# Kernel tuning notes

Measured on AMD Instinct MI355X. Metric: run time of the kernel, lower is better.

## Reference

```python
import jax, jax.numpy as jnp
import numpy as np

CODEBOOK_SIZE = 8192
D_MODEL = 256
COMMITMENT_COST = 0.25


def setup_inputs() -> dict:
    key = jax.random.key(0)
    k1, k2 = jax.random.split(key)
    z = jax.random.normal(k1, (16, 512, D_MODEL), dtype=jnp.float32)
    # uniform(-1/K, 1/K) init like the torch module
    codebook = jax.random.uniform(
        k2, (CODEBOOK_SIZE, D_MODEL), dtype=jnp.float32,
        minval=-1.0 / CODEBOOK_SIZE, maxval=1.0 / CODEBOOK_SIZE)
    return {"z": z, "codebook": codebook}


def reference(z, codebook):
    B, P, D = z.shape
    flat = z.reshape(-1, D)  # [N, D]
    distances = (jnp.sum(flat * flat, axis=1, keepdims=True)
                 + jnp.sum(codebook * codebook, axis=1)
                 - 2.0 * jnp.matmul(flat, codebook.T))
    indices = jnp.argmin(distances, axis=1)  # [N] int
    quantized = codebook[indices]            # [N, D] gather
    # non-EMA VQ loss: codebook loss + commitment loss
    e_latent_loss = jnp.mean((jax.lax.stop_gradient(quantized) - flat) ** 2)
    q_latent_loss = jnp.mean((quantized - jax.lax.stop_gradient(flat)) ** 2)
    loss = q_latent_loss + COMMITMENT_COST * e_latent_loss
    # straight-through estimator
    quantized_st = flat + jax.lax.stop_gradient(quantized - flat)
    return (loss, quantized_st.reshape(B, P, D), indices.reshape(B, P))
```

## Files before the change

### kernel.cpp

```cpp
#include <hip/hip_runtime.h>
#include <hip/hip_bf16.h>
#include <math.h>


#define NROWS 8192
#define DDIM  256
#define KCW   8192
#define CAP   128
#define MARGIN 5e-4f

typedef __attribute__((ext_vector_type(8))) short short8;
typedef __attribute__((ext_vector_type(4))) float f32x4;
typedef unsigned int u32;

__device__ inline void async_copy16(void* lds_uniform, const void* gsrc) {
  __builtin_amdgcn_global_load_lds(
      (const __attribute__((address_space(1))) u32*)gsrc,
      (__attribute__((address_space(3))) u32*)lds_uniform, 16, 0, 0);
}

__device__ inline unsigned fmap(float f) {
  unsigned b = __float_as_uint(f);
  return (b & 0x80000000u) ? ~b : (b | 0x80000000u);
}
__device__ inline float funmap(unsigned u) {
  unsigned b = (u & 0x80000000u) ? (u & 0x7FFFFFFFu) : ~u;
  return __uint_as_float(b);
}

__global__ __launch_bounds__(256) void k_prep_cast(const float* __restrict__ z,
                                                   const float* __restrict__ cb,
                                                   ushort* __restrict__ zb,
                                                   ushort* __restrict__ cbb,
                                                   float* __restrict__ e2f,
                                                   unsigned* __restrict__ rowMinU,
                                                   unsigned* __restrict__ cnt) {
  int t = threadIdx.x, w = t >> 6, lane = t & 63;
  int wid = blockIdx.x * 4 + w;
  bool isCb = wid >= NROWS;
  int row = isCb ? wid - NROWS : wid;
  const float* src = (isCb ? cb : z) + (size_t)row * DDIM + lane * 4;
  float4 v = *reinterpret_cast<const float4*>(src);
  ushort4 o;
  __hip_bfloat16 bx = __float2bfloat16(v.x); o.x = *(ushort*)&bx;
  __hip_bfloat16 by = __float2bfloat16(v.y); o.y = *(ushort*)&by;
  __hip_bfloat16 bz = __float2bfloat16(v.z); o.z = *(ushort*)&bz;
  __hip_bfloat16 bw = __float2bfloat16(v.w); o.w = *(ushort*)&bw;
  ushort* dst = (isCb ? cbb : zb) + (size_t)row * DDIM + lane * 4;
  *reinterpret_cast<ushort4*>(dst) = o;
  if (isCb) {
    double d = (double)v.x * v.x + (double)v.y * v.y + (double)v.z * v.z + (double)v.w * v.w;
#pragma unroll
    for (int off = 1; off < 64; off <<= 1) d += __shfl_xor(d, off);
    if (lane == 0) e2f[row] = (float)d;
  } else {
    if (lane == 0) { rowMinU[row] = ~0u; cnt[row] = 0; }
  }
}

__global__ __launch_bounds__(256) void k_score1(const ushort* __restrict__ zb,
                                                const ushort* __restrict__ cbb,
                                                const float* __restrict__ e2f,
                                                unsigned* __restrict__ rowMinU,
                                                unsigned* __restrict__ cnt,
                                                ushort* __restrict__ cand) {
  __shared__ ushort Ab[128 * 64];
  __shared__ ushort Bb[128 * 64];
  int t = threadIdx.x, w = t >> 6, lane = t & 63;
  int wg = ((blockIdx.x & 7) << 9) | (blockIdx.x >> 3);
  int mt = wg >> 6, nt = wg & 63;
  int wm = w >> 1, wn = w & 1;
  int cl = lane & 15, g = lane >> 4;

  int rloc8 = lane >> 3;
  int sslot = (lane & 7) ^ rloc8;
  const ushort* arow_base = zb  + (size_t)(mt * 128) * DDIM;
  const ushort* brow_base = cbb + (size_t)(nt * 128) * DDIM;

  f32x4 acc[4][4];
#pragma unroll
  for (int m = 0; m < 4; ++m)
#pragma unroll
    for (int n = 0; n < 4; ++n) acc[m][n] = (f32x4){0.f, 0.f, 0.f, 0.f};

  for (int ks = 0; ks < 4; ++ks) {
#pragma unroll
    for (int i = 0; i < 8; ++i) {
      int ch = w * 8 + i;
      int ct = ch & 15;
      int row = ct * 8 + rloc8;
      const ushort* src = (ch < 16)
          ? arow_base + (size_t)row * DDIM + ks * 64 + sslot * 8
          : brow_base + (size_t)row * DDIM + ks * 64 + sslot * 8;
      char* ldsb = (char*)(ch < 16 ? Ab : Bb) + ct * 1024;
      async_copy16(ldsb, src);
    }
    __syncthreads();
#pragma unroll
    for (int kk = 0; kk < 2; ++kk) {
      short8 af[4], bf[4];
#pragma unroll
      for (int m = 0; m < 4; ++m) {
        int arow = wm * 64 + m * 16 + cl;
        int ab = arow * 128 + (((kk * 4 + g) ^ (arow & 7)) << 4);
        af[m] = *reinterpret_cast<const short8*>((char*)Ab + ab);
      }
#pragma unroll
      for (int n = 0; n < 4; ++n) {
        int brow = wn * 64 + n * 16 + cl;
        int bb = brow * 128 + (((kk * 4 + g) ^ (brow & 7)) << 4);
        bf[n] = *reinterpret_cast<const short8*>((char*)Bb + bb);
      }
#pragma unroll
      for (int m = 0; m < 4; ++m)
#pragma unroll
        for (int n = 0; n < 4; ++n)
          acc[m][n] = __builtin_amdgcn_mfma_f32_16x16x32_bf16(af[m], bf[n], acc[m][n], 0, 0, 0);
    }
    __syncthreads();
  }

  int col_base = nt * 128 + wn * 64;
  int row_base = mt * 128 + wm * 64;
  float e2v[4];
#pragma unroll
  for (int n = 0; n < 4; ++n) e2v[n] = e2f[col_base + n * 16 + cl];

#pragma unroll
  for (int m = 0; m < 4; ++m) {
#pragma unroll
    for (int j = 0; j < 4; ++j) {
      int row = row_base + m * 16 + g * 4 + j;
      float s0 = __fsub_rn(e2v[0], __fmul_rn(2.0f, acc[m][0][j]));
      float s1 = __fsub_rn(e2v[1], __fmul_rn(2.0f, acc[m][1][j]));
      float s2 = __fsub_rn(e2v[2], __fmul_rn(2.0f, acc[m][2][j]));
      float s3 = __fsub_rn(e2v[3], __fmul_rn(2.0f, acc[m][3][j]));
      float mn = fminf(fminf(s0, s1), fminf(s2, s3));
#pragma unroll
      for (int off = 1; off < 16; off <<= 1)
        mn = fminf(mn, __shfl_xor(mn, off));
      float thr;
      if (cl == 0) {
        unsigned old = atomicMin(&rowMinU[row], fmap(mn));
        thr = fminf(funmap(old), mn) + MARGIN;
      }
      thr = __shfl(thr, g << 4);
      if (s0 <= thr) { unsigned sl = atomicAdd(&cnt[row], 1u); if (sl < CAP) cand[(size_t)row * CAP + sl] = (ushort)(col_base + 0 * 16 + cl); }
      if (s1 <= thr) { unsigned sl = atomicAdd(&cnt[row], 1u); if (sl < CAP) cand[(size_t)row * CAP + sl] = (ushort)(col_base + 1 * 16 + cl); }
      if (s2 <= thr) { unsigned sl = atomicAdd(&cnt[row], 1u); if (sl < CAP) cand[(size_t)row * CAP + sl] = (ushort)(col_base + 2 * 16 + cl); }
      if (s3 <= thr) { unsigned sl = atomicAdd(&cnt[row], 1u); if (sl < CAP) cand[(size_t)row * CAP + sl] = (ushort)(col_base + 3 * 16 + cl); }
    }
  }
}

__global__ __launch_bounds__(256) void k_rescore_gather(const float* __restrict__ z,
                                                        const float* __restrict__ cb,
                                                        const float* __restrict__ e2f,
                                                        const unsigned* __restrict__ cnt,
                                                        const ushort* __restrict__ cand,
                                                        float* __restrict__ out_q,
                                                        float* __restrict__ out_idx,
                                                        float* __restrict__ lpart) {
  int t = threadIdx.x, w = t >> 6, lane = t & 63;
  int row = blockIdx.x * 4 + w;
  const float* xp = z + (size_t)row * DDIM;
  const float4* xp4 = reinterpret_cast<const float4*>(xp);
  float4 x4 = xp4[lane];
  double rd = (double)x4.x * x4.x + (double)x4.y * x4.y + (double)x4.z * x4.z + (double)x4.w * x4.w;
#pragma unroll
  for (int off = 1; off < 64; off <<= 1) rd += __shfl_xor(rd, off);
  float r2v = (float)rd;

  unsigned n = cnt[row];
  float s = INFINITY; int ci = 0x7fffffff;
  if (n <= CAP) {
#pragma unroll
    for (int base = 0; base < CAP; base += 64) {
      int k_i = base + lane;
      if (k_i < (int)n) {
        int c = cand[(size_t)row * CAP + k_i];
        const float4* ep4 = reinterpret_cast<const float4*>(cb + (size_t)c * DDIM);
        float acc = 0.f;
#pragma unroll 4
        for (int k4 = 0; k4 < 64; ++k4) {
          float4 e = ep4[k4], x = xp4[k4];
          acc = __fmaf_rn(x.x, e.x, acc);
          acc = __fmaf_rn(x.y, e.y, acc);
          acc = __fmaf_rn(x.z, e.z, acc);
          acc = __fmaf_rn(x.w, e.w, acc);
        }
        float scv = __fsub_rn(__fadd_rn(r2v, e2f[c]), __fmul_rn(2.0f, acc));
        if (scv < s || (scv == s && c < ci)) { s = scv; ci = c; }
      }
    }
  } else {
    for (int base = 0; base < KCW; base += 64) {
      int c = base + lane;
      const float4* ep4 = reinterpret_cast<const float4*>(cb + (size_t)c * DDIM);
      float acc = 0.f;
#pragma unroll 4
      for (int k4 = 0; k4 < 64; ++k4) {
        float4 e = ep4[k4], x = xp4[k4];
        acc = __fmaf_rn(x.x, e.x, acc);
        acc = __fmaf_rn(x.y, e.y, acc);
        acc = __fmaf_rn(x.z, e.z, acc);
        acc = __fmaf_rn(x.w, e.w, acc);
      }
      float scv = __fsub_rn(__fadd_rn(r2v, e2f[c]), __fmul_rn(2.0f, acc));
      if (scv < s) { s = scv; ci = c; }
    }
  }
#pragma unroll
  for (int off = 1; off < 64; off <<= 1) {
    float os = __shfl_xor(s, off); int oi = __shfl_xor(ci, off);
    if (os < s || (os == s && oi < ci)) { s = os; ci = oi; }
  }
  if (lane == 0) out_idx[row] = (float)ci;

  float4 qv = *reinterpret_cast<const float4*>(cb + (size_t)ci * DDIM + lane * 4);
  float* o = out_q + (size_t)row * DDIM + lane * 4;
  o[0] = qv.x; o[1] = qv.y; o[2] = qv.z; o[3] = qv.w;
  float dx = qv.x - x4.x, dy = qv.y - x4.y, dz = qv.z - x4.z, dw = qv.w - x4.w;
  double d = (double)dx * dx + (double)dy * dy + (double)dz * dz + (double)dw * dw;
#pragma unroll
  for (int off = 1; off < 64; off <<= 1) d += __shfl_xor(d, off);
  if (lane == 0) lpart[row] = (float)d;
}

__global__ __launch_bounds__(256) void k_loss(const float* __restrict__ lpart,
                                              float* __restrict__ out0) {
  __shared__ double red[256];
  int t = threadIdx.x;
  double s = 0.0;
  for (int j = t; j < NROWS; j += 256) s += lpart[j];
  red[t] = s;
  __syncthreads();
  for (int off = 128; off > 0; off >>= 1) {
    if (t < off) red[t] += red[t + off];
    __syncthreads();
  }
  if (t == 0) out0[0] = (float)(1.25 * red[0] / (double)((size_t)NROWS * DDIM));
}

extern "C" void kernel_launch(void* const* d_in, const int* in_sizes, int n_in,
                              void* d_out, int out_size, void* d_ws, size_t ws_size,
                              hipStream_t stream) {
  const float* z  = (const float*)d_in[0];
  const float* cb = (const float*)d_in[1];
  float* out = (float*)d_out;
  char* ws = (char*)d_ws;
  const size_t HALF = (size_t)NROWS * DDIM;

  ushort* zb  = (ushort*)(out + 4);
  ushort* cbb = zb + HALF;

  size_t off = 0;
  float*    e2f     = (float*)(ws + off);    off += NROWS * 4;
  unsigned* cnt     = (unsigned*)(ws + off); off += NROWS * 4;
  unsigned* rowMinU = (unsigned*)(ws + off);
  float*    lpart   = (float*)(ws + off);    off += NROWS * 4;
  ushort*   cand    = (ushort*)(ws + off);   off += (size_t)NROWS * CAP * 2;

  float* out_q   = out + 1;
  float* out_idx = out + 1 + HALF;

  k_prep_cast     <<<(2 * NROWS) / 4, 256, 0, stream>>>(z, cb, zb, cbb, e2f, rowMinU, cnt);
  k_score1        <<<64 * 64,         256, 0, stream>>>(zb, cbb, e2f, rowMinU, cnt, cand);
  k_rescore_gather<<<NROWS / 4,       256, 0, stream>>>(z, cb, e2f, cnt, cand, out_q, out_idx, lpart);
  k_loss          <<<1,               256, 0, stream>>>(lpart, out);
}
```

Before: 246.3 us.

## Split scoring into exact-min pass and candidate-filter pass to shrink rescore work

Replaces the single scoring kernel, which used a running atomic minimum, with two passes over the bf16 distance GEMM. The first pass computes each row's exact approximate minimum and the second collects only candidates within a margin of it. This gives far fewer candidates, so the cap drops to 56 and the fp32 rescore runs as a single per-lane pass. The K-tile also grows to 128 with larger LDS buffers and launch bounds of 2. The cost is running the GEMM twice, in exchange for less atomic contention and a much cheaper rescore.

```diff
diff --git a/kernel.cpp b/kernel.cpp
--- a/kernel.cpp
+++ b/kernel.cpp
@@ -6,8 +6,8 @@
 #define NROWS 8192
 #define DDIM  256
 #define KCW   8192
-#define CAP   128
-#define MARGIN 5e-4f
+#define CAP   56
+#define MARGIN 8e-4f
 
 typedef __attribute__((ext_vector_type(8))) short short8;
 typedef __attribute__((ext_vector_type(4))) float f32x4;
@@ -54,26 +54,27 @@
     for (int off = 1; off < 64; off <<= 1) d += __shfl_xor(d, off);
     if (lane == 0) e2f[row] = (float)d;
   } else {
-    if (lane == 0) { rowMinU[row] = ~0u; cnt[row] = 0; }
-  }
-}
-
-__global__ __launch_bounds__(256) void k_score1(const ushort* __restrict__ zb,
-                                                const ushort* __restrict__ cbb,
-                                                const float* __restrict__ e2f,
-                                                unsigned* __restrict__ rowMinU,
-                                                unsigned* __restrict__ cnt,
-                                                ushort* __restrict__ cand) {
-  __shared__ ushort Ab[128 * 64];
-  __shared__ ushort Bb[128 * 64];
+    if (lane == 0) { rowMinU[row] = 0xFF800000u; cnt[row] = 0; }
+  }
+}
+
+template<int PHASE>
+__global__ __launch_bounds__(256, 2) void k_score(const ushort* __restrict__ zb,
+                                                  const ushort* __restrict__ cbb,
+                                                  const float* __restrict__ e2f,
+                                                  unsigned* __restrict__ rowMinU,
+                                                  unsigned* __restrict__ cnt,
+                                                  int* __restrict__ cand) {
+  __shared__ ushort Ab[128 * 128];
+  __shared__ ushort Bb[128 * 128];
   int t = threadIdx.x, w = t >> 6, lane = t & 63;
   int wg = ((blockIdx.x & 7) << 9) | (blockIdx.x >> 3);
   int mt = wg >> 6, nt = wg & 63;
   int wm = w >> 1, wn = w & 1;
   int cl = lane & 15, g = lane >> 4;
 
-  int rloc8 = lane >> 3;
-  int sslot = (lane & 7) ^ rloc8;
+  int rloc4 = lane >> 4;
+  int slot  = lane & 15;
   const ushort* arow_base = zb  + (size_t)(mt * 128) * DDIM;
   const ushort* brow_base = cbb + (size_t)(nt * 128) * DDIM;
 
@@ -83,32 +84,33 @@
 #pragma unroll
     for (int n = 0; n < 4; ++n) acc[m][n] = (f32x4){0.f, 0.f, 0.f, 0.f};
 
-  for (int ks = 0; ks < 4; ++ks) {
-#pragma unroll
-    for (int i = 0; i < 8; ++i) {
-      int ch = w * 8 + i;
-      int ct = ch & 15;
-      int row = ct * 8 + rloc8;
-      const ushort* src = (ch < 16)
-          ? arow_base + (size_t)row * DDIM + ks * 64 + sslot * 8
-          : brow_base + (size_t)row * DDIM + ks * 64 + sslot * 8;
-      char* ldsb = (char*)(ch < 16 ? Ab : Bb) + ct * 1024;
+  for (int ks = 0; ks < 2; ++ks) {
+#pragma unroll
+    for (int i = 0; i < 16; ++i) {
+      int ch = w * 16 + i;
+      bool isA = ch < 32;
+      int ct = isA ? ch : ch - 32;
+      int rowc = ct * 4 + rloc4;
+      int ss = slot ^ (rowc & 7);
+      const ushort* src = (isA ? arow_base : brow_base)
+                          + (size_t)rowc * DDIM + ks * 128 + ss * 8;
+      char* ldsb = (char*)(isA ? Ab : Bb) + ct * 1024;
       async_copy16(ldsb, src);
     }
     __syncthreads();
 #pragma unroll
-    for (int kk = 0; kk < 2; ++kk) {
+    for (int kk = 0; kk < 4; ++kk) {
       short8 af[4], bf[4];
 #pragma unroll
       for (int m = 0; m < 4; ++m) {
         int arow = wm * 64 + m * 16 + cl;
-        int ab = arow * 128 + (((kk * 4 + g) ^ (arow & 7)) << 4);
+        int ab = arow * 256 + (((kk * 4 + g) ^ (arow & 7)) << 4);
         af[m] = *reinterpret_cast<const short8*>((char*)Ab + ab);
       }
 #pragma unroll
       for (int n = 0; n < 4; ++n) {
         int brow = wn * 64 + n * 16 + cl;
-        int bb = brow * 128 + (((kk * 4 + g) ^ (brow & 7)) << 4);
+        int bb = brow * 256 + (((kk * 4 + g) ^ (brow & 7)) << 4);
         bf[n] = *reinterpret_cast<const short8*>((char*)Bb + bb);
       }
 #pragma unroll
@@ -131,24 +133,28 @@
 #pragma unroll
     for (int j = 0; j < 4; ++j) {
       int row = row_base + m * 16 + g * 4 + j;
-      float s0 = __fsub_rn(e2v[0], __fmul_rn(2.0f, acc[m][0][j]));
-      float s1 = __fsub_rn(e2v[1], __fmul_rn(2.0f, acc[m][1][j]));
-      float s2 = __fsub_rn(e2v[2], __fmul_rn(2.0f, acc[m][2][j]));
-      float s3 = __fsub_rn(e2v[3], __fmul_rn(2.0f, acc[m][3][j]));
-      float mn = fminf(fminf(s0, s1), fminf(s2, s3));
-#pragma unroll
-      for (int off = 1; off < 16; off <<= 1)
-        mn = fminf(mn, __shfl_xor(mn, off));
-      float thr;
-      if (cl == 0) {
-        unsigned old = atomicMin(&rowMinU[row], fmap(mn));
-        thr = fminf(funmap(old), mn) + MARGIN;
-      }
-      thr = __shfl(thr, g << 4);
-      if (s0 <= thr) { unsigned sl = atomicAdd(&cnt[row], 1u); if (sl < CAP) cand[(size_t)row * CAP + sl] = (ushort)(col_base + 0 * 16 + cl); }
-      if (s1 <= thr) { unsigned sl = atomicAdd(&cnt[row], 1u); if (sl < CAP) cand[(size_t)row * CAP + sl] = (ushort)(col_base + 1 * 16 + cl); }
-      if (s2 <= thr) { unsigned sl = atomicAdd(&cnt[row], 1u); if (sl < CAP) cand[(size_t)row * CAP + sl] = (ushort)(col_base + 2 * 16 + cl); }
-      if (s3 <= thr) { unsigned sl = atomicAdd(&cnt[row], 1u); if (sl < CAP) cand[(size_t)row * CAP + sl] = (ushort)(col_base + 3 * 16 + cl); }
+      if (PHASE == 1) {
+        float mn = INFINITY;
+#pragma unroll
+        for (int n = 0; n < 4; ++n) {
+          float s = __fsub_rn(e2v[n], __fmul_rn(2.0f, acc[m][n][j]));
+          mn = fminf(mn, s);
+        }
+#pragma unroll
+        for (int off = 1; off < 16; off <<= 1)
+          mn = fminf(mn, __shfl_xor(mn, off));
+        if (cl == 0) atomicMin(&rowMinU[row], fmap(mn));
+      } else {
+        float thr = funmap(rowMinU[row]) + MARGIN;
+#pragma unroll
+        for (int n = 0; n < 4; ++n) {
+          float s = __fsub_rn(e2v[n], __fmul_rn(2.0f, acc[m][n][j]));
+          if (s <= thr) {
+            unsigned sl = atomicAdd(&cnt[row], 1u);
+            if (sl < CAP) cand[row * CAP + sl] = col_base + n * 16 + cl;
+          }
+        }
+      }
     }
   }
 }
@@ -157,7 +163,7 @@
                                                         const float* __restrict__ cb,
                                                         const float* __restrict__ e2f,
                                                         const unsigned* __restrict__ cnt,
-                                                        const ushort* __restrict__ cand,
+                                                        const int* __restrict__ cand,
                                                         float* __restrict__ out_q,
                                                         float* __restrict__ out_idx,
                                                         float* __restrict__ lpart) {
@@ -174,24 +180,19 @@
   unsigned n = cnt[row];
   float s = INFINITY; int ci = 0x7fffffff;
   if (n <= CAP) {
-#pragma unroll
-    for (int base = 0; base < CAP; base += 64) {
-      int k_i = base + lane;
-      if (k_i < (int)n) {
-        int c = cand[(size_t)row * CAP + k_i];
-        const float4* ep4 = reinterpret_cast<const float4*>(cb + (size_t)c * DDIM);
-        float acc = 0.f;
+    if (lane < (int)n) {
+      ci = cand[row * CAP + lane];
+      const float4* ep4 = reinterpret_cast<const float4*>(cb + (size_t)ci * DDIM);
+      float acc = 0.f;
 #pragma unroll 4
-        for (int k4 = 0; k4 < 64; ++k4) {
-          float4 e = ep4[k4], x = xp4[k4];
-          acc = __fmaf_rn(x.x, e.x, acc);
-          acc = __fmaf_rn(x.y, e.y, acc);
-          acc = __fmaf_rn(x.z, e.z, acc);
-          acc = __fmaf_rn(x.w, e.w, acc);
-        }
-        float scv = __fsub_rn(__fadd_rn(r2v, e2f[c]), __fmul_rn(2.0f, acc));
-        if (scv < s || (scv == s && c < ci)) { s = scv; ci = c; }
-      }
+      for (int k4 = 0; k4 < 64; ++k4) {
+        float4 e = ep4[k4], x = xp4[k4];
+        acc = __fmaf_rn(x.x, e.x, acc);
+        acc = __fmaf_rn(x.y, e.y, acc);
+        acc = __fmaf_rn(x.z, e.z, acc);
+        acc = __fmaf_rn(x.w, e.w, acc);
+      }
+      s = __fsub_rn(__fadd_rn(r2v, e2f[ci]), __fmul_rn(2.0f, acc));
     }
   } else {
     for (int base = 0; base < KCW; base += 64) {
@@ -259,13 +260,14 @@
   unsigned* cnt     = (unsigned*)(ws + off); off += NROWS * 4;
   unsigned* rowMinU = (unsigned*)(ws + off);
   float*    lpart   = (float*)(ws + off);    off += NROWS * 4;
-  ushort*   cand    = (ushort*)(ws + off);   off += (size_t)NROWS * CAP * 2;
+  int*      cand    = (int*)(ws + off);      off += (size_t)NROWS * CAP * 4;
 
   float* out_q   = out + 1;
   float* out_idx = out + 1 + HALF;
 
   k_prep_cast     <<<(2 * NROWS) / 4, 256, 0, stream>>>(z, cb, zb, cbb, e2f, rowMinU, cnt);
-  k_score1        <<<64 * 64,         256, 0, stream>>>(zb, cbb, e2f, rowMinU, cnt, cand);
+  k_score<1>      <<<64 * 64,         256, 0, stream>>>(zb, cbb, e2f, rowMinU, cnt, cand);
+  k_score<2>      <<<64 * 64,         256, 0, stream>>>(zb, cbb, e2f, rowMinU, cnt, cand);
   k_rescore_gather<<<NROWS / 4,       256, 0, stream>>>(z, cb, e2f, cnt, cand, out_q, out_idx, lpart);
   k_loss          <<<1,               256, 0, stream>>>(lpart, out);
 }
```

After: 236.0 us. 1.04x faster.
